# Kernel optimization log

Measured on AMD Instinct MI355X. Metric: run time of the kernel, lower is better.

## Reference

```python
import jax, jax.numpy as jnp
import numpy as np

B, S, D = 8, 2048, 2048
E, R, K = 8, 16, 2
NUM_TASKS, NUM_MODES = 4, 2
ALPHA = 16.0


def setup_inputs() -> dict:
    key = jax.random.key(0)
    k1, k2, k3, k4 = jax.random.split(key, 4)
    hidden_states = jax.random.normal(k1, (B, S, D), dtype=jnp.float32)
    gate_w = jax.random.normal(k2, (E, D), dtype=jnp.float32) * 0.01  # nn.init.normal_(std=0.01)
    # Soft-prior biases: fill(-1.0), strong prior 3.0 / 2.0 at configured (task, expert) / (mode, expert)
    tb = -np.ones((NUM_TASKS, E), dtype=np.float32)
    mb = -np.ones((NUM_MODES, E), dtype=np.float32)
    for e in range(E):
        tb[e % NUM_TASKS, e] = 3.0
        mb[e % NUM_MODES, e] = 2.0
    # LoRA params; lora_B is zero-init in torch but we use small random values for a nontrivial baseline
    lora_A = jax.random.normal(k3, (E, R, D), dtype=jnp.float32) * (1.0 / np.sqrt(D))
    lora_B = jax.random.normal(k4, (E, D, R), dtype=jnp.float32) * 0.02
    return {
        "hidden_states": hidden_states,
        "gate_w": gate_w,
        "task_bias": jnp.asarray(tb),
        "mode_bias": jnp.asarray(mb),
        "lora_A": lora_A,
        "lora_B": lora_B,
        "task_id": 1,
        "mode_id": 1,
    }


def reference(hidden_states, gate_w, task_bias, mode_bias, lora_A, lora_B, task_id, mode_id):
    scaling = ALPHA / R
    # Router: score = dynamic_gate(mean_pool(x)) + task_bias[t] + mode_bias[m]
    x_pooled = hidden_states.mean(axis=1)                       # [B, D]
    logits = x_pooled @ gate_w.T + task_bias[task_id] + mode_bias[mode_id]  # [B, E]
    top_v, top_i = jax.lax.top_k(logits, K)                     # [B, K]
    weights = jax.nn.softmax(top_v, axis=-1)                    # [B, K]
    # per-sample, per-expert combine weight: sum of top-k weights routed to that expert
    one_hot = jax.nn.one_hot(top_i, E, dtype=weights.dtype)     # [B, K, E]
    sw = jnp.einsum('bke,bk->be', one_hot, weights)             # [B, E]
    # LoRA experts: (x @ A_e^T) @ B_e^T * scaling, weighted-summed per sample
    mid = jnp.einsum('bsd,erd->besr', hidden_states, lora_A)    # [B, E, S, R] (small: R=16)
    out = jnp.einsum('be,besr,edr->bsd', sw, mid, lora_B) * scaling  # [B, S, D]
    return out
```

## Files before the change

### kernel.cpp

```cpp
#include <hip/hip_runtime.h>
#include <stdint.h>

typedef __attribute__((ext_vector_type(8))) short bf16x8;
typedef __attribute__((ext_vector_type(4))) float f32x4;
typedef __attribute__((ext_vector_type(16))) float f32x16;
typedef unsigned short ushort_t;

#define B_ 8
#define S_ 2048
#define D_ 2048
#define E_ 8
#define J_ 128
#define AROWS 160
#define ATILE (AROWS * 64)

static __device__ __forceinline__ unsigned short f2bf(float f) {
  union { float f; uint32_t u; } v; v.f = f;
  uint32_t u = v.u;
  return (unsigned short)((u + 0x7FFFu + ((u >> 16) & 1u)) >> 16);
}
static __device__ __forceinline__ float bf2f(ushort_t h) {
  union { uint32_t u; float f; } v; v.u = ((uint32_t)h) << 16;
  return v.f;
}
static __device__ __forceinline__ uint32_t pkbf(float a, float b) {
  uint32_t r;
  asm("v_cvt_pk_bf16_f32 %0, %1, %2" : "=v"(r) : "v"(a), "v"(b));
  return r;
}

#define GLL16(gsrc, ldst)                                                        \
  __builtin_amdgcn_global_load_lds(                                              \
      (const __attribute__((address_space(1))) void*)(gsrc),                     \
      (__attribute__((address_space(3))) void*)(ldst), 16, 0, 0)

#define VMBAR(N)                                                                 \
  do {                                                                           \
    asm volatile("s_waitcnt vmcnt(" #N ") lgkmcnt(0)\n\ts_barrier" ::: "memory");\
    __builtin_amdgcn_sched_barrier(0);                                           \
  } while (0)

__global__ void k_prep(const float* __restrict__ lA, const float* __restrict__ lB,
                       const float* __restrict__ gw,
                       ushort_t* __restrict__ AgE, ushort_t* __restrict__ Bg) {
  int gid = blockIdx.x * blockDim.x + threadIdx.x;
  int stride = gridDim.x * blockDim.x;
  for (int o = gid; o < 32 * AROWS * 8; o += stride) {
    int kt = o / (AROWS * 8);
    int rem = o - kt * (AROWS * 8);
    int row = rem >> 3, c = rem & 7;
    int d = kt * 64 + (((c ^ row) & 7) << 3);
    bf16x8 outv = {};
    if (row < 136) {
      const float* src = (row < 128) ? (lA + (size_t)row * D_ + d)
                                     : (gw + (size_t)(row - 128) * D_ + d);
      float4 v0 = *(const float4*)src;
      float4 v1 = *(const float4*)(src + 4);
      outv[0] = (short)f2bf(v0.x); outv[1] = (short)f2bf(v0.y);
      outv[2] = (short)f2bf(v0.z); outv[3] = (short)f2bf(v0.w);
      outv[4] = (short)f2bf(v1.x); outv[5] = (short)f2bf(v1.y);
      outv[6] = (short)f2bf(v1.z); outv[7] = (short)f2bf(v1.w);
    }
    *(bf16x8*)&AgE[(size_t)o * 8] = outv;
  }
  for (int o4 = gid; o4 < (D_ * J_) / 4; o4 += stride) {
    int j4 = o4 & 31, dd = o4 >> 5;
    int e = j4 >> 2, r0 = (j4 & 3) * 4;
    float4 v = *(const float4*)(lB + ((size_t)e * D_ + dd) * 16 + r0);
    uint2 pk;
    pk.x = (uint32_t)f2bf(v.x) | ((uint32_t)f2bf(v.y) << 16);
    pk.y = (uint32_t)f2bf(v.z) | ((uint32_t)f2bf(v.w) << 16);
    ((uint2*)Bg)[o4] = pk;
  }
}

__global__ __launch_bounds__(256) void k_mid(const float* __restrict__ x,
    const ushort_t* __restrict__ AgE, ushort_t* __restrict__ midb,
    float* __restrict__ lpart) {
  __shared__ ushort_t Ab[2][ATILE];
  __shared__ ushort_t Xb[2][2048];
  const int tid = threadIdx.x;
  const int w = tid >> 6, lane = tid & 63;
  const int l31 = lane & 31, hi = lane >> 5;
  const int b = blockIdx.y, s0 = blockIdx.x * 32;
  const float* xb = x + ((size_t)(b * S_ + s0)) * D_;
  const int xr = tid >> 4, xc = (tid & 15) * 4;
  const float* xsrc0 = xb + (size_t)xr * D_ + xc;
  const float* xsrc1 = xb + (size_t)(16 + xr) * D_ + xc;
  const int xw0 = xr * 64 + ((((xc >> 3) ^ (xr & 7))) << 3) + ((xc >> 2) & 1) * 4;
  const int xw1 = (16 + xr) * 64 + ((((xc >> 3) ^ ((16 + xr) & 7))) << 3) + ((xc >> 2) & 1) * 4;

  f32x16 acc = {};
  f32x16 acc2 = {};

  auto stageA = [&](int buf, int kt) {
#pragma unroll
    for (int c = 0; c < 5; ++c) {
      int ch = c * 256 + tid;
      const ushort_t* src = AgE + (size_t)kt * ATILE + (size_t)ch * 8;
      GLL16(src, &Ab[buf][ch * 8]);
    }
  };
  auto loadX = [&](float4* xr4, int t) {
    xr4[0] = *(const float4*)(xsrc0 + t * 64);
    xr4[1] = *(const float4*)(xsrc1 + t * 64);
  };
  auto cvtWrite = [&](int buf, const float4* xr4) {
    uint2 p0, p1;
    p0.x = pkbf(xr4[0].x, xr4[0].y); p0.y = pkbf(xr4[0].z, xr4[0].w);
    p1.x = pkbf(xr4[1].x, xr4[1].y); p1.y = pkbf(xr4[1].z, xr4[1].w);
    *(uint2*)&Xb[buf][xw0] = p0;
    *(uint2*)&Xb[buf][xw1] = p1;
  };
  auto computeTile = [&](int t) {
    const int cb = t & 1;
#pragma unroll
    for (int ks = 0; ks < 4; ++ks) {
      const int cc = ks * 2 + hi;
      bf16x8 xf = *(const bf16x8*)&Xb[cb][l31 * 64 + ((cc ^ (l31 & 7)) << 3)];
      const int arow = w * 32 + l31;
      bf16x8 af = *(const bf16x8*)&Ab[cb][arow * 64 + ((cc ^ (l31 & 7)) << 3)];
      acc = __builtin_amdgcn_mfma_f32_32x32x16_bf16(af, xf, acc, 0, 0, 0);
      if (w == 3) {
        const int arow2 = 128 + l31;
        bf16x8 af2 = *(const bf16x8*)&Ab[cb][arow2 * 64 + ((cc ^ (l31 & 7)) << 3)];
        acc2 = __builtin_amdgcn_mfma_f32_32x32x16_bf16(af2, xf, acc2, 0, 0, 0);
      }
    }
  };

  float4 xA[2], xB[2];
  stageA(0, 0);
  __builtin_amdgcn_sched_barrier(0);
  loadX(xA, 0);
  cvtWrite(0, xA);
  loadX(xB, 1);
  __builtin_amdgcn_sched_barrier(0);

#pragma unroll 1
  for (int tt = 0; tt < 15; ++tt) {
    const int t = 2 * tt;
    VMBAR(2);
    stageA((t + 1) & 1, t + 1);
    cvtWrite((t + 1) & 1, xB);
    loadX(xA, t + 2);
    computeTile(t);
    VMBAR(2);
    stageA(t & 1, t + 2);
    cvtWrite(t & 1, xA);
    loadX(xB, t + 3);
    computeTile(t + 1);
  }
  VMBAR(2);
  stageA(1, 31);
  cvtWrite(1, xB);
  computeTile(30);
  VMBAR(0);
  computeTile(31);

  {
    ushort_t* mp = midb + ((size_t)(b * S_ + s0 + l31)) * J_ + w * 32 + 4 * hi;
#pragma unroll
    for (int G = 0; G < 4; ++G) {
      uint2 pk;
      pk.x = pkbf(acc[G * 4 + 0], acc[G * 4 + 1]);
      pk.y = pkbf(acc[G * 4 + 2], acc[G * 4 + 3]);
      *(uint2*)&mp[G * 8] = pk;
    }
  }

  if (w == 3) {
    float lsq[4];
#pragma unroll
    for (int q = 0; q < 4; ++q) {
      float v = acc2[q];
      v += __shfl_xor(v, 1); v += __shfl_xor(v, 2);
      v += __shfl_xor(v, 4); v += __shfl_xor(v, 8);
      v += __shfl_xor(v, 16);
      lsq[q] = v;
    }
    if (l31 == 0) {
      float* lp = lpart + ((size_t)(b * 64 + blockIdx.x)) * 8 + hi * 4;
      lp[0] = lsq[0]; lp[1] = lsq[1]; lp[2] = lsq[2]; lp[3] = lsq[3];
    }
  }
}

__global__ void k_router(const float* __restrict__ lpart,
                         const float* __restrict__ tb, const float* __restrict__ mb,
                         const int* __restrict__ task_p, const int* __restrict__ mode_p,
                         float* __restrict__ rinfo) {
  __shared__ float lg[64];
  const int t = threadIdx.x;
  const int b = t >> 3, e = t & 7;
  float s = 0.f;
  for (int k = 0; k < 64; ++k) s += lpart[((size_t)(b * 64 + k)) * 8 + e];
  lg[t] = s * (1.f / (float)S_) + tb[task_p[0] * E_ + e] + mb[mode_p[0] * E_ + e];
  __syncthreads();
  if (t < B_) {
    float v[8];
#pragma unroll
    for (int e2 = 0; e2 < 8; ++e2) v[e2] = lg[t * 8 + e2];
    int i1 = 0;
#pragma unroll
    for (int e2 = 1; e2 < 8; ++e2) if (v[e2] > v[i1]) i1 = e2;
    int i2 = (i1 == 0) ? 1 : 0;
#pragma unroll
    for (int e2 = 0; e2 < 8; ++e2) if (e2 != i1 && v[e2] > v[i2]) i2 = e2;
    float ex = __expf(v[i2] - v[i1]);
    float w1 = 1.f / (1.f + ex), w2 = ex * w1;
    float4 r;
    r.x = (float)i1; r.y = (float)i2; r.z = w1; r.w = w2;
    ((float4*)rinfo)[t] = r;
  }
}

__global__ __launch_bounds__(256) void k_comb(const ushort_t* __restrict__ midb,
    const float* __restrict__ rinfo, const ushort_t* __restrict__ Bg,
    float* __restrict__ out) {
  __shared__ ushort_t Bt[128][40];
  const int n = blockIdx.x, m = blockIdx.y, b = blockIdx.z;
  const int tid = threadIdx.x, w = tid >> 6, lane = tid & 63;
  const int lm = lane & 15, g = lane >> 4;

  const float4 ri = ((const float4*)rinfo)[b];
  const int i1 = (int)ri.x, i2 = (int)ri.y;
  const float w1 = ri.z, w2 = ri.w;

#pragma unroll
  for (int c = 0; c < 2; ++c) {
    int ci = c * 256 + tid;
    int d = ci >> 2, sub = ci & 3;
    int e = (sub & 2) ? i2 : i1;
    float sc = (sub & 2) ? w2 : w1;
    bf16x8 bv = *(const bf16x8*)(Bg + ((size_t)(n * 128 + d)) * J_ + e * 16 + (sub & 1) * 8);
    bf16x8 bw;
#pragma unroll
    for (int i = 0; i < 8; ++i) bw[i] = (short)f2bf(bf2f((ushort_t)bv[i]) * sc);
    *(bf16x8*)&Bt[d][sub * 8] = bw;
  }

  const int srow = m * 64 + w * 16 + lm;
  const int jw = (g < 2) ? (i1 * 16 + g * 8) : (i2 * 16 + (g - 2) * 8);
  bf16x8 pf = *(const bf16x8*)&midb[((size_t)(b * S_ + srow)) * J_ + jw];
  __syncthreads();

  f32x4 acc[8] = {};
#pragma unroll
  for (int nn = 0; nn < 8; ++nn) {
    bf16x8 af = *(const bf16x8*)&Bt[nn * 16 + lm][g * 8];
    acc[nn] = __builtin_amdgcn_mfma_f32_16x16x32_bf16(af, pf, acc[nn], 0, 0, 0);
  }

  float* op = out + ((size_t)(b * S_ + srow)) * D_ + n * 128;
#pragma unroll
  for (int nn = 0; nn < 8; ++nn)
    *(f32x4*)&op[nn * 16 + g * 4] = acc[nn];
}

extern "C" void kernel_launch(void* const* d_in, const int* in_sizes, int n_in,
                              void* d_out, int out_size, void* d_ws, size_t ws_size,
                              hipStream_t stream) {
  const float* x    = (const float*)d_in[0];
  const float* gw   = (const float*)d_in[1];
  const float* tb   = (const float*)d_in[2];
  const float* mb   = (const float*)d_in[3];
  const float* lA   = (const float*)d_in[4];
  const float* lB   = (const float*)d_in[5];
  const int* task_p = (const int*)d_in[6];
  const int* mode_p = (const int*)d_in[7];
  float* out = (float*)d_out;
  char* ws = (char*)d_ws;
  ushort_t* midb = (ushort_t*)ws;
  ushort_t* AgE  = (ushort_t*)(ws + 4194304);
  ushort_t* Bg   = (ushort_t*)(ws + 4849664);
  float* lpart   = (float*)(ws + 5373952);
  float* rinfo   = (float*)(ws + 5390336);

  hipLaunchKernelGGL(k_prep, dim3(256), dim3(256), 0, stream, lA, lB, gw, AgE, Bg);
  hipLaunchKernelGGL(k_mid, dim3(64, 8), dim3(256), 0, stream, x, AgE, midb, lpart);
  hipLaunchKernelGGL(k_router, dim3(1), dim3(64), 0, stream,
                     lpart, tb, mb, task_p, mode_p, rinfo);
  hipLaunchKernelGGL(k_comb, dim3(16, 32, 8), dim3(256), 0, stream, midb, rinfo, Bg, out);
}
```

Measured before the change: 85.26 us.

## Triple-buffer weight tiles with deeper X prefetch and trim padded rows

Trims the padded weight tile from 160 to 136 rows, so each stage loads fewer bytes and the layout buffer shrinks. It moves the k_mid pipeline from double to triple buffering of the A tiles and prefetches X two tiles ahead, with explicit vmcnt waits and sched barriers. The goal is to hide global-load latency better behind the MFMA work. In exchange it uses more LDS, which may lower occupancy, and the wait counts become more fragile.

Measured after the change: 87.13 us. 2.2% more time.

```diff
diff --git a/kernel.cpp b/kernel.cpp
--- a/kernel.cpp
+++ b/kernel.cpp
@@ -11,7 +11,7 @@
 #define D_ 2048
 #define E_ 8
 #define J_ 128
-#define AROWS 160
+#define AROWS 136
 #define ATILE (AROWS * 64)
 
 static __device__ __forceinline__ unsigned short f2bf(float f) {
@@ -33,6 +33,8 @@
   __builtin_amdgcn_global_load_lds(                                              \
       (const __attribute__((address_space(1))) void*)(gsrc),                     \
       (__attribute__((address_space(3))) void*)(ldst), 16, 0, 0)
+
+#define SBAR() __builtin_amdgcn_sched_barrier(0)
 
 #define VMBAR(N)                                                                 \
   do {                                                                           \
@@ -50,17 +52,15 @@
     int rem = o - kt * (AROWS * 8);
     int row = rem >> 3, c = rem & 7;
     int d = kt * 64 + (((c ^ row) & 7) << 3);
-    bf16x8 outv = {};
-    if (row < 136) {
-      const float* src = (row < 128) ? (lA + (size_t)row * D_ + d)
-                                     : (gw + (size_t)(row - 128) * D_ + d);
-      float4 v0 = *(const float4*)src;
-      float4 v1 = *(const float4*)(src + 4);
-      outv[0] = (short)f2bf(v0.x); outv[1] = (short)f2bf(v0.y);
-      outv[2] = (short)f2bf(v0.z); outv[3] = (short)f2bf(v0.w);
-      outv[4] = (short)f2bf(v1.x); outv[5] = (short)f2bf(v1.y);
-      outv[6] = (short)f2bf(v1.z); outv[7] = (short)f2bf(v1.w);
-    }
+    const float* src = (row < 128) ? (lA + (size_t)row * D_ + d)
+                                   : (gw + (size_t)(row - 128) * D_ + d);
+    float4 v0 = *(const float4*)src;
+    float4 v1 = *(const float4*)(src + 4);
+    bf16x8 outv;
+    outv[0] = (short)f2bf(v0.x); outv[1] = (short)f2bf(v0.y);
+    outv[2] = (short)f2bf(v0.z); outv[3] = (short)f2bf(v0.w);
+    outv[4] = (short)f2bf(v1.x); outv[5] = (short)f2bf(v1.y);
+    outv[6] = (short)f2bf(v1.z); outv[7] = (short)f2bf(v1.w);
     *(bf16x8*)&AgE[(size_t)o * 8] = outv;
   }
   for (int o4 = gid; o4 < (D_ * J_) / 4; o4 += stride) {
@@ -77,7 +77,7 @@
 __global__ __launch_bounds__(256) void k_mid(const float* __restrict__ x,
     const ushort_t* __restrict__ AgE, ushort_t* __restrict__ midb,
     float* __restrict__ lpart) {
-  __shared__ ushort_t Ab[2][ATILE];
+  __shared__ ushort_t Ab[3][ATILE];
   __shared__ ushort_t Xb[2][2048];
   const int tid = threadIdx.x;
   const int w = tid >> 6, lane = tid & 63;
@@ -95,10 +95,15 @@
 
   auto stageA = [&](int buf, int kt) {
 #pragma unroll
-    for (int c = 0; c < 5; ++c) {
+    for (int c = 0; c < 4; ++c) {
       int ch = c * 256 + tid;
       const ushort_t* src = AgE + (size_t)kt * ATILE + (size_t)ch * 8;
       GLL16(src, &Ab[buf][ch * 8]);
+    }
+    {
+      int ch = 1024 + lane;
+      const ushort_t* src = AgE + (size_t)kt * ATILE + (size_t)ch * 8;
+      GLL16(src, &Ab[buf][(1024 + (tid & 63)) * 8]);
     }
   };
   auto loadX = [&](float4* xr4, int t) {
@@ -112,51 +117,85 @@
     *(uint2*)&Xb[buf][xw0] = p0;
     *(uint2*)&Xb[buf][xw1] = p1;
   };
-  auto computeTile = [&](int t) {
+  auto computeTile = [&](int t, int ab) {
     const int cb = t & 1;
 #pragma unroll
     for (int ks = 0; ks < 4; ++ks) {
       const int cc = ks * 2 + hi;
       bf16x8 xf = *(const bf16x8*)&Xb[cb][l31 * 64 + ((cc ^ (l31 & 7)) << 3)];
       const int arow = w * 32 + l31;
-      bf16x8 af = *(const bf16x8*)&Ab[cb][arow * 64 + ((cc ^ (l31 & 7)) << 3)];
+      bf16x8 af = *(const bf16x8*)&Ab[ab][arow * 64 + ((cc ^ (l31 & 7)) << 3)];
       acc = __builtin_amdgcn_mfma_f32_32x32x16_bf16(af, xf, acc, 0, 0, 0);
       if (w == 3) {
         const int arow2 = 128 + l31;
-        bf16x8 af2 = *(const bf16x8*)&Ab[cb][arow2 * 64 + ((cc ^ (l31 & 7)) << 3)];
+        bf16x8 af2 = *(const bf16x8*)&Ab[ab][arow2 * 64 + ((cc ^ (l31 & 7)) << 3)];
         acc2 = __builtin_amdgcn_mfma_f32_32x32x16_bf16(af2, xf, acc2, 0, 0, 0);
       }
     }
   };
 
-  float4 xA[2], xB[2];
-  stageA(0, 0);
-  __builtin_amdgcn_sched_barrier(0);
-  loadX(xA, 0);
-  cvtWrite(0, xA);
-  loadX(xB, 1);
-  __builtin_amdgcn_sched_barrier(0);
-
+  float4 xR0[2], xR1[2], xR2[2];
+  loadX(xR0, 0); loadX(xR1, 1); loadX(xR2, 2);
+  SBAR();
+  stageA(0, 0); stageA(1, 1);
+  SBAR();
+  cvtWrite(0, xR0);
+  SBAR();
+
+  {
+    VMBAR(5);
+    stageA(2, 2); SBAR();
+    cvtWrite(1, xR1); SBAR();
+    loadX(xR0, 3); SBAR();
+    computeTile(0, 0);
+  }
+  {
+    VMBAR(7);
+    stageA(0, 3); SBAR();
+    cvtWrite(0, xR2); SBAR();
+    loadX(xR1, 4); SBAR();
+    computeTile(1, 1);
+  }
 #pragma unroll 1
-  for (int tt = 0; tt < 15; ++tt) {
-    const int t = 2 * tt;
-    VMBAR(2);
-    stageA((t + 1) & 1, t + 1);
-    cvtWrite((t + 1) & 1, xB);
-    loadX(xA, t + 2);
-    computeTile(t);
-    VMBAR(2);
-    stageA(t & 1, t + 2);
-    cvtWrite(t & 1, xA);
-    loadX(xB, t + 3);
-    computeTile(t + 1);
-  }
-  VMBAR(2);
-  stageA(1, 31);
-  cvtWrite(1, xB);
-  computeTile(30);
-  VMBAR(0);
-  computeTile(31);
+  for (int k3 = 0; k3 < 9; ++k3) {
+    const int t = 3 * k3 + 2;
+    {
+      VMBAR(9);
+      stageA(1, t + 2); SBAR();
+      cvtWrite((t + 1) & 1, xR0); SBAR();
+      loadX(xR2, t + 3); SBAR();
+      computeTile(t, 2);
+    }
+    {
+      VMBAR(9);
+      stageA(2, t + 3); SBAR();
+      cvtWrite((t + 2) & 1, xR1); SBAR();
+      loadX(xR0, t + 4); SBAR();
+      computeTile(t + 1, 0);
+    }
+    {
+      VMBAR(9);
+      stageA(0, t + 4); SBAR();
+      cvtWrite((t + 3) & 1, xR2); SBAR();
+      loadX(xR1, t + 5); SBAR();
+      computeTile(t + 2, 1);
+    }
+  }
+  {
+    VMBAR(9);
+    stageA(1, 31); SBAR();
+    cvtWrite(0, xR0); SBAR();
+    computeTile(29, 2);
+  }
+  {
+    VMBAR(7);
+    cvtWrite(1, xR1); SBAR();
+    computeTile(30, 0);
+  }
+  {
+    VMBAR(0);
+    computeTile(31, 1);
+  }
 
   {
     ushort_t* mp = midb + ((size_t)(b * S_ + s0 + l31)) * J_ + w * 32 + 4 * hi;
@@ -273,9 +312,9 @@
   char* ws = (char*)d_ws;
   ushort_t* midb = (ushort_t*)ws;
   ushort_t* AgE  = (ushort_t*)(ws + 4194304);
-  ushort_t* Bg   = (ushort_t*)(ws + 4849664);
-  float* lpart   = (float*)(ws + 5373952);
-  float* rinfo   = (float*)(ws + 5390336);
+  ushort_t* Bg   = (ushort_t*)(ws + 4751360);
+  float* lpart   = (float*)(ws + 5275648);
+  float* rinfo   = (float*)(ws + 5292032);
 
   hipLaunchKernelGGL(k_prep, dim3(256), dim3(256), 0, stream, lA, lB, gw, AgE, Bg);
   hipLaunchKernelGGL(k_mid, dim3(64, 8), dim3(256), 0, stream, x, AgE, midb, lpart);
```

## Double sequence tile per block in k_mid and triple-buffer expert weight tiles

Applied to the files above, without the earlier changes.

k_mid now handles 64 sequence rows per block instead of 32, so each staged LoRA-A/gate weight tile serves twice as many rows and the grid halves to 32x8 blocks. The A tile drops its padding rows (160 to 136), and A staging becomes a three-buffer pipeline with loads issued two tiles ahead. Each wave now computes two 32x32 MFMA accumulators, with the gate-logit MFMA moved to the even waves. The goal is less global and LDS traffic for the weights and better latency hiding on the x stream, at the cost of more registers per thread, more LDS, and fewer blocks in flight.

Result: faster. 80.19 us (-5.9%).

```diff
diff --git a/kernel.cpp b/kernel.cpp
--- a/kernel.cpp
+++ b/kernel.cpp
@@ -11,7 +11,8 @@
 #define D_ 2048
 #define E_ 8
 #define J_ 128
-#define AROWS 160
+#define M_ 64
+#define AROWS 136
 #define ATILE (AROWS * 64)
 
 static __device__ __forceinline__ unsigned short f2bf(float f) {
@@ -34,6 +35,12 @@
       (const __attribute__((address_space(1))) void*)(gsrc),                     \
       (__attribute__((address_space(3))) void*)(ldst), 16, 0, 0)
 
+#define SBAR() __builtin_amdgcn_sched_barrier(0)
+#define VMWAIT(N)                                                                \
+  do {                                                                           \
+    asm volatile("s_waitcnt vmcnt(" #N ")" ::: "memory");                        \
+    __builtin_amdgcn_sched_barrier(0);                                           \
+  } while (0)
 #define VMBAR(N)                                                                 \
   do {                                                                           \
     asm volatile("s_waitcnt vmcnt(" #N ") lgkmcnt(0)\n\ts_barrier" ::: "memory");\
@@ -50,17 +57,15 @@
     int rem = o - kt * (AROWS * 8);
     int row = rem >> 3, c = rem & 7;
     int d = kt * 64 + (((c ^ row) & 7) << 3);
-    bf16x8 outv = {};
-    if (row < 136) {
-      const float* src = (row < 128) ? (lA + (size_t)row * D_ + d)
-                                     : (gw + (size_t)(row - 128) * D_ + d);
-      float4 v0 = *(const float4*)src;
-      float4 v1 = *(const float4*)(src + 4);
-      outv[0] = (short)f2bf(v0.x); outv[1] = (short)f2bf(v0.y);
-      outv[2] = (short)f2bf(v0.z); outv[3] = (short)f2bf(v0.w);
-      outv[4] = (short)f2bf(v1.x); outv[5] = (short)f2bf(v1.y);
-      outv[6] = (short)f2bf(v1.z); outv[7] = (short)f2bf(v1.w);
-    }
+    const float* src = (row < 128) ? (lA + (size_t)row * D_ + d)
+                                   : (gw + (size_t)(row - 128) * D_ + d);
+    float4 v0 = *(const float4*)src;
+    float4 v1 = *(const float4*)(src + 4);
+    bf16x8 outv;
+    outv[0] = (short)f2bf(v0.x); outv[1] = (short)f2bf(v0.y);
+    outv[2] = (short)f2bf(v0.z); outv[3] = (short)f2bf(v0.w);
+    outv[4] = (short)f2bf(v1.x); outv[5] = (short)f2bf(v1.y);
+    outv[6] = (short)f2bf(v1.z); outv[7] = (short)f2bf(v1.w);
     *(bf16x8*)&AgE[(size_t)o * 8] = outv;
   }
   for (int o4 = gid; o4 < (D_ * J_) / 4; o4 += stride) {
@@ -77,111 +82,128 @@
 __global__ __launch_bounds__(256) void k_mid(const float* __restrict__ x,
     const ushort_t* __restrict__ AgE, ushort_t* __restrict__ midb,
     float* __restrict__ lpart) {
-  __shared__ ushort_t Ab[2][ATILE];
-  __shared__ ushort_t Xb[2][2048];
+  __shared__ ushort_t Ab[3][ATILE];
+  __shared__ ushort_t Xb[2][M_ * 64];
   const int tid = threadIdx.x;
   const int w = tid >> 6, lane = tid & 63;
   const int l31 = lane & 31, hi = lane >> 5;
-  const int b = blockIdx.y, s0 = blockIdx.x * 32;
-  const float* xb = x + ((size_t)(b * S_ + s0)) * D_;
-  const int xr = tid >> 4, xc = (tid & 15) * 4;
-  const float* xsrc0 = xb + (size_t)xr * D_ + xc;
-  const float* xsrc1 = xb + (size_t)(16 + xr) * D_ + xc;
-  const int xw0 = xr * 64 + ((((xc >> 3) ^ (xr & 7))) << 3) + ((xc >> 2) & 1) * 4;
-  const int xw1 = (16 + xr) * 64 + ((((xc >> 3) ^ ((16 + xr) & 7))) << 3) + ((xc >> 2) & 1) * 4;
-
-  f32x16 acc = {};
-  f32x16 acc2 = {};
+  const int jp = w & 1, sp = w >> 1;
+  const int b = blockIdx.y, s0 = blockIdx.x * M_;
+  const int xr = tid >> 2, xc4 = (tid & 3) * 16;
+  const float* xsrc = x + ((size_t)(b * S_ + s0 + xr)) * D_ + xc4;
+  const int lc0 = 2 * (tid & 3);
+
+  f32x16 accA = {}, accB = {}, acc2 = {};
 
   auto stageA = [&](int buf, int kt) {
 #pragma unroll
-    for (int c = 0; c < 5; ++c) {
+    for (int c = 0; c < 4; ++c) {
       int ch = c * 256 + tid;
-      const ushort_t* src = AgE + (size_t)kt * ATILE + (size_t)ch * 8;
-      GLL16(src, &Ab[buf][ch * 8]);
+      GLL16(AgE + (size_t)kt * ATILE + (size_t)ch * 8, &Ab[buf][ch * 8]);
+    }
+    {
+      int ch = 1024 + lane;
+      GLL16(AgE + (size_t)kt * ATILE + (size_t)ch * 8, &Ab[buf][(1024 + lane) * 8]);
     }
   };
-  auto loadX = [&](float4* xr4, int t) {
-    xr4[0] = *(const float4*)(xsrc0 + t * 64);
-    xr4[1] = *(const float4*)(xsrc1 + t * 64);
+  auto loadX = [&](float4* r4, int t) {
+    const float* p = xsrc + t * 64;
+    r4[0] = *(const float4*)(p);
+    r4[1] = *(const float4*)(p + 4);
+    r4[2] = *(const float4*)(p + 8);
+    r4[3] = *(const float4*)(p + 12);
   };
-  auto cvtWrite = [&](int buf, const float4* xr4) {
-    uint2 p0, p1;
-    p0.x = pkbf(xr4[0].x, xr4[0].y); p0.y = pkbf(xr4[0].z, xr4[0].w);
-    p1.x = pkbf(xr4[1].x, xr4[1].y); p1.y = pkbf(xr4[1].z, xr4[1].w);
-    *(uint2*)&Xb[buf][xw0] = p0;
-    *(uint2*)&Xb[buf][xw1] = p1;
+  auto cvtWrite = [&](int buf, const float4* r4) {
+    uint4 q0, q1;
+    q0.x = pkbf(r4[0].x, r4[0].y); q0.y = pkbf(r4[0].z, r4[0].w);
+    q0.z = pkbf(r4[1].x, r4[1].y); q0.w = pkbf(r4[1].z, r4[1].w);
+    q1.x = pkbf(r4[2].x, r4[2].y); q1.y = pkbf(r4[2].z, r4[2].w);
+    q1.z = pkbf(r4[3].x, r4[3].y); q1.w = pkbf(r4[3].z, r4[3].w);
+    const int ph0 = lc0 ^ (xr & 7), ph1 = (lc0 + 1) ^ (xr & 7);
+    *(uint4*)&Xb[buf][xr * 64 + ph0 * 8] = q0;
+    *(uint4*)&Xb[buf][xr * 64 + ph1 * 8] = q1;
   };
-  auto computeTile = [&](int t) {
-    const int cb = t & 1;
+  auto computeTile = [&](int t, int ab) {
+    const int xbuf = t & 1;
+    const int xrow = sp * 32 + l31;
+    const int a0 = jp * 64 + l31, a1 = jp * 64 + 32 + l31, a2 = 128 + l31;
+    const int rsw = (l31 & 7);
 #pragma unroll
     for (int ks = 0; ks < 4; ++ks) {
       const int cc = ks * 2 + hi;
-      bf16x8 xf = *(const bf16x8*)&Xb[cb][l31 * 64 + ((cc ^ (l31 & 7)) << 3)];
-      const int arow = w * 32 + l31;
-      bf16x8 af = *(const bf16x8*)&Ab[cb][arow * 64 + ((cc ^ (l31 & 7)) << 3)];
-      acc = __builtin_amdgcn_mfma_f32_32x32x16_bf16(af, xf, acc, 0, 0, 0);
-      if (w == 3) {
-        const int arow2 = 128 + l31;
-        bf16x8 af2 = *(const bf16x8*)&Ab[cb][arow2 * 64 + ((cc ^ (l31 & 7)) << 3)];
+      const int chs = ((cc ^ rsw) << 3);
+      bf16x8 xf = *(const bf16x8*)&Xb[xbuf][xrow * 64 + chs];
+      bf16x8 af0 = *(const bf16x8*)&Ab[ab][a0 * 64 + chs];
+      bf16x8 af1 = *(const bf16x8*)&Ab[ab][a1 * 64 + chs];
+      accA = __builtin_amdgcn_mfma_f32_32x32x16_bf16(af0, xf, accA, 0, 0, 0);
+      accB = __builtin_amdgcn_mfma_f32_32x32x16_bf16(af1, xf, accB, 0, 0, 0);
+      if ((w & 1) == 0) {
+        bf16x8 af2 = *(const bf16x8*)&Ab[ab][a2 * 64 + chs];
         acc2 = __builtin_amdgcn_mfma_f32_32x32x16_bf16(af2, xf, acc2, 0, 0, 0);
       }
     }
   };
 
-  float4 xA[2], xB[2];
-  stageA(0, 0);
-  __builtin_amdgcn_sched_barrier(0);
-  loadX(xA, 0);
-  cvtWrite(0, xA);
-  loadX(xB, 1);
-  __builtin_amdgcn_sched_barrier(0);
+  float4 xS0[4], xS1[4];
+  loadX(xS0, 0); SBAR();
+  stageA(0, 0);  SBAR();
+  loadX(xS1, 1); SBAR();
+  stageA(1, 1);  SBAR();
+  VMWAIT(14);
+  cvtWrite(0, xS0);
+  VMBAR(9);
+
+#define BODY(T, AB, ABN, XCUR, XNXT)                                             \
+  do {                                                                           \
+    loadX(XNXT, (T) + 2); SBAR();                                                \
+    stageA((ABN), (T) + 2); SBAR();                                              \
+    computeTile((T), (AB));                                                      \
+    VMWAIT(14);                                                                  \
+    cvtWrite(((T) + 1) & 1, XCUR);                                               \
+    VMBAR(9);                                                                    \
+  } while (0)
 
 #pragma unroll 1
-  for (int tt = 0; tt < 15; ++tt) {
-    const int t = 2 * tt;
-    VMBAR(2);
-    stageA((t + 1) & 1, t + 1);
-    cvtWrite((t + 1) & 1, xB);
-    loadX(xA, t + 2);
-    computeTile(t);
-    VMBAR(2);
-    stageA(t & 1, t + 2);
-    cvtWrite(t & 1, xA);
-    loadX(xB, t + 3);
-    computeTile(t + 1);
-  }
-  VMBAR(2);
-  stageA(1, 31);
-  cvtWrite(1, xB);
-  computeTile(30);
+  for (int k6 = 0; k6 < 5; ++k6) {
+    const int t0 = 6 * k6;
+    BODY(t0 + 0, 0, 2, xS1, xS0);
+    BODY(t0 + 1, 1, 0, xS0, xS1);
+    BODY(t0 + 2, 2, 1, xS1, xS0);
+    BODY(t0 + 3, 0, 2, xS0, xS1);
+    BODY(t0 + 4, 1, 0, xS1, xS0);
+    BODY(t0 + 5, 2, 1, xS0, xS1);
+  }
+#undef BODY
+  computeTile(30, 0);
+  VMWAIT(5);
+  cvtWrite(1, xS1);
   VMBAR(0);
-  computeTile(31);
+  computeTile(31, 1);
 
   {
-    ushort_t* mp = midb + ((size_t)(b * S_ + s0 + l31)) * J_ + w * 32 + 4 * hi;
+    const int srow = s0 + sp * 32 + l31;
+    ushort_t* mp = midb + ((size_t)(b * S_ + srow)) * J_ + jp * 64 + 4 * hi;
 #pragma unroll
     for (int G = 0; G < 4; ++G) {
-      uint2 pk;
-      pk.x = pkbf(acc[G * 4 + 0], acc[G * 4 + 1]);
-      pk.y = pkbf(acc[G * 4 + 2], acc[G * 4 + 3]);
-      *(uint2*)&mp[G * 8] = pk;
-    }
-  }
-
-  if (w == 3) {
-    float lsq[4];
+      uint2 pA, pB;
+      pA.x = pkbf(accA[G * 4 + 0], accA[G * 4 + 1]);
+      pA.y = pkbf(accA[G * 4 + 2], accA[G * 4 + 3]);
+      pB.x = pkbf(accB[G * 4 + 0], accB[G * 4 + 1]);
+      pB.y = pkbf(accB[G * 4 + 2], accB[G * 4 + 3]);
+      *(uint2*)&mp[G * 8] = pA;
+      *(uint2*)&mp[32 + G * 8] = pB;
+    }
+  }
+
+  if ((w & 1) == 0) {
 #pragma unroll
     for (int q = 0; q < 4; ++q) {
       float v = acc2[q];
       v += __shfl_xor(v, 1); v += __shfl_xor(v, 2);
       v += __shfl_xor(v, 4); v += __shfl_xor(v, 8);
       v += __shfl_xor(v, 16);
-      lsq[q] = v;
-    }
-    if (l31 == 0) {
-      float* lp = lpart + ((size_t)(b * 64 + blockIdx.x)) * 8 + hi * 4;
-      lp[0] = lsq[0]; lp[1] = lsq[1]; lp[2] = lsq[2]; lp[3] = lsq[3];
+      if (l31 == 0)
+        lpart[(((size_t)(b * 32 + blockIdx.x)) * 2 + sp) * 8 + hi * 4 + q] = v;
     }
   }
 }
@@ -273,12 +295,12 @@
   char* ws = (char*)d_ws;
   ushort_t* midb = (ushort_t*)ws;
   ushort_t* AgE  = (ushort_t*)(ws + 4194304);
-  ushort_t* Bg   = (ushort_t*)(ws + 4849664);
-  float* lpart   = (float*)(ws + 5373952);
-  float* rinfo   = (float*)(ws + 5390336);
+  ushort_t* Bg   = (ushort_t*)(ws + 4751360);
+  float* lpart   = (float*)(ws + 5275648);
+  float* rinfo   = (float*)(ws + 5292032);
 
   hipLaunchKernelGGL(k_prep, dim3(256), dim3(256), 0, stream, lA, lB, gw, AgE, Bg);
-  hipLaunchKernelGGL(k_mid, dim3(64, 8), dim3(256), 0, stream, x, AgE, midb, lpart);
+  hipLaunchKernelGGL(k_mid, dim3(32, 8), dim3(256), 0, stream, x, AgE, midb, lpart);
   hipLaunchKernelGGL(k_router, dim3(1), dim3(64), 0, stream,
                      lpart, tb, mb, task_p, mode_p, rinfo);
   hipLaunchKernelGGL(k_comb, dim3(16, 32, 8), dim3(256), 0, stream, midb, rinfo, Bg, out);
```
